# Kernel tuning notes

Hardware: AMD Instinct MI355X
Metric: run time of the kernel (lower is better)

Reference implementation:

```python
import jax, jax.numpy as jnp
from jax import lax
import numpy as np
import math

T, B, F = 512, 256, 256  # num_steps, batch, input_size == hidden_size
H = F


def setup_inputs() -> dict:
    key = jax.random.key(0)
    ks = jax.random.split(key, 20)
    stdv = 1.0 / math.sqrt(H)

    def u(k, n):
        return jax.random.uniform(k, (n,), jnp.float32, -stdv, stdv)

    X = jax.random.normal(ks[0], (T, B, F), jnp.float32)
    Mask = (jax.random.uniform(ks[1], (T, B, F)) < 0.7).astype(jnp.float32)
    Delta = jax.random.uniform(ks[2], (T, B, F), jnp.float32)

    return {
        "X": X, "Mask": Mask, "Delta": Delta,
        "x_mean": u(ks[3], F),
        "w_dg_x": u(ks[4], F), "b_dg_x": u(ks[5], F),
        "w_dg_h": u(ks[6], H), "b_dg_h": u(ks[7], H),
        "w_xz": u(ks[8], F), "u_hz": u(ks[9], H), "b_z": u(ks[10], H),
        "w_xr": u(ks[11], F), "u_hr": u(ks[12], H), "b_r": u(ks[13], H),
        "w_xh": u(ks[14], F), "u_hh": u(ks[15], H), "v_mh": u(ks[16], F),
        "b_h": u(ks[17], H),
    }


def reference(X, Mask, Delta, x_mean, w_dg_x, b_dg_x, w_dg_h, b_dg_h,
              w_xz, u_hz, b_z, w_xr, u_hr, b_r, w_xh, u_hh, v_mh, b_h):
    batch = X.shape[1]

    def step(h, inp):
        x, m, d = inp  # each [B, F]
        gamma_x = jnp.exp(-jnp.maximum(0.0, w_dg_x * d + b_dg_x))
        gamma_h = jnp.exp(-jnp.maximum(0.0, w_dg_h * d + b_dg_h))
        x = m * x + (1.0 - m) * (gamma_x * x + (1.0 - gamma_x) * x_mean)
        h = gamma_h * h
        z = jax.nn.sigmoid(w_xz * x + u_hz * h + b_z)
        r = jax.nn.sigmoid(w_xr * x + u_hr * h + b_r)
        h_tilde = jnp.tanh(w_xh * x + u_hh * (r * h) + v_mh * m + b_h)
        h = (1.0 - z) * h + z * h_tilde
        return h, h

    h0 = jnp.zeros((batch, H), X.dtype)
    _, hs = lax.scan(step, h0, (X, Mask, Delta))  # hs: [T, B, H]
    hidden_states = jnp.transpose(hs, (1, 0, 2))  # [B, T, H]
    return hidden_states, hidden_states[:, -1, :]
```

## Files before the change

### kernel.cpp

```cpp
#include <hip/hip_runtime.h>
#include <math.h>


#define TT 512
#define BB 256
#define FF 256
#define BF (BB * FF)
#define CH 8
#define NCH (TT / CH)

__device__ __forceinline__ float fast_sigmoid(float x) {
    return __builtin_amdgcn_rcpf(1.0f + __expf(-x));
}
__device__ __forceinline__ float fast_tanh(float x) {
    return fmaf(-2.0f, __builtin_amdgcn_rcpf(1.0f + __expf(2.0f * x)), 1.0f);
}

__global__ __launch_bounds__(512) void grud_kernel(
    const float* __restrict__ X, const float* __restrict__ Mask,
    const float* __restrict__ Delta,
    const float* __restrict__ x_mean,
    const float* __restrict__ w_dg_x, const float* __restrict__ b_dg_x,
    const float* __restrict__ w_dg_h, const float* __restrict__ b_dg_h,
    const float* __restrict__ w_xz, const float* __restrict__ u_hz,
    const float* __restrict__ b_z,
    const float* __restrict__ w_xr, const float* __restrict__ u_hr,
    const float* __restrict__ b_r,
    const float* __restrict__ w_xh, const float* __restrict__ u_hh,
    const float* __restrict__ v_mh, const float* __restrict__ b_h,
    float* __restrict__ out)
{
    __shared__ float lds[2][3][CH][FF];

    const int tid = threadIdx.x;
    const int blk = blockIdx.x;

    if (tid >= 256) {
        const int j = tid - 256;
        const float* srcs[3] = { X     + (size_t)blk * FF,
                                 Mask  + (size_t)blk * FF,
                                 Delta + (size_t)blk * FF };

        {
            #pragma unroll
            for (int arr = 0; arr < 3; ++arr) {
                const float* s = srcs[arr];
                #pragma unroll
                for (int i2 = 0; i2 < 2; ++i2) {
                    const int rem  = i2 * 256 + j;
                    const int step = rem >> 6;
                    const int f4   = (rem & 63) << 2;
                    *(float4*)&lds[0][arr][step][f4] =
                        *(const float4*)(s + (size_t)step * BF + f4);
                }
            }
        }
        __syncthreads();

        for (int k = 0; k < NCH; ++k) {
            if (k + 1 < NCH) {
                const int bufi = (k + 1) & 1;
                const int t0   = (k + 1) * CH;
                #pragma unroll
                for (int arr = 0; arr < 3; ++arr) {
                    const float* s = srcs[arr];
                    #pragma unroll
                    for (int i2 = 0; i2 < 2; ++i2) {
                        const int rem  = i2 * 256 + j;
                        const int step = rem >> 6;
                        const int f4   = (rem & 63) << 2;
                        *(float4*)&lds[bufi][arr][step][f4] =
                            *(const float4*)(s + (size_t)(t0 + step) * BF + f4);
                    }
                }
            }
            __syncthreads();
        }
    } else {
        const int f = tid;
        const float xm  = x_mean[f];
        const float wdx = w_dg_x[f], bdx = b_dg_x[f];
        const float wdh = w_dg_h[f], bdh = b_dg_h[f];
        const float wxz = w_xz[f],   uhz = u_hz[f], bz = b_z[f];
        const float wxr = w_xr[f],   uhr = u_hr[f], br = b_r[f];
        const float wxh = w_xh[f],   uhh = u_hh[f];
        const float vmh = v_mh[f],   bh  = b_h[f];

        float h = 0.0f;
        __syncthreads();

        for (int k = 0; k < NCH; ++k) {
            const int cb = k & 1;
            float* op = out + ((size_t)blk * TT + (size_t)k * CH) * FF + f;
            #pragma unroll
            for (int s = 0; s < CH; ++s) {
                float x = lds[cb][0][s][f];
                float m = lds[cb][1][s][f];
                float d = lds[cb][2][s][f];

                float gx = __expf(-fmaxf(0.0f, fmaf(wdx, d, bdx)));
                float gh = __expf(-fmaxf(0.0f, fmaf(wdh, d, bdh)));
                float xhat = fmaf(gx, x, (1.0f - gx) * xm);
                x = fmaf(m, x, (1.0f - m) * xhat);
                h = gh * h;
                float z  = fast_sigmoid(fmaf(wxz, x, fmaf(uhz, h, bz)));
                float r  = fast_sigmoid(fmaf(wxr, x, fmaf(uhr, h, br)));
                float ht = fast_tanh(fmaf(wxh, x, fmaf(uhh, r * h, fmaf(vmh, m, bh))));
                h = fmaf(z, ht - h, h);
                op[s * FF] = h;
            }
            __syncthreads();
        }

        out[(size_t)BB * TT * FF + (size_t)blk * FF + f] = h;
    }
}

extern "C" void kernel_launch(void* const* d_in, const int* in_sizes, int n_in,
                              void* d_out, int out_size, void* d_ws, size_t ws_size,
                              hipStream_t stream) {
    const float* X      = (const float*)d_in[0];
    const float* Mask   = (const float*)d_in[1];
    const float* Delta  = (const float*)d_in[2];
    const float* x_mean = (const float*)d_in[3];
    const float* w_dg_x = (const float*)d_in[4];
    const float* b_dg_x = (const float*)d_in[5];
    const float* w_dg_h = (const float*)d_in[6];
    const float* b_dg_h = (const float*)d_in[7];
    const float* w_xz   = (const float*)d_in[8];
    const float* u_hz   = (const float*)d_in[9];
    const float* b_z    = (const float*)d_in[10];
    const float* w_xr   = (const float*)d_in[11];
    const float* u_hr   = (const float*)d_in[12];
    const float* b_r    = (const float*)d_in[13];
    const float* w_xh   = (const float*)d_in[14];
    const float* u_hh   = (const float*)d_in[15];
    const float* v_mh   = (const float*)d_in[16];
    const float* b_h    = (const float*)d_in[17];
    float* out = (float*)d_out;

    grud_kernel<<<BB, 512, 0, stream>>>(
        X, Mask, Delta, x_mean, w_dg_x, b_dg_x, w_dg_h, b_dg_h,
        w_xz, u_hz, b_z, w_xr, u_hr, b_r, w_xh, u_hh, v_mh, b_h, out);
}
```

Before: 412.2 us.

## Replace LDS producer warps with register double-buffered direct loads

Drops the producer/consumer split that staged X/Mask/Delta through double-buffered LDS with block barriers. Each thread now loads its own feature column for two chunks of 16 steps into register arrays and alternates compute and prefetch, with no barriers. Outputs are written with nontemporal stores. This removes LDS traffic and __syncthreads, but the loads become scalar per-thread accesses (still coalesced across the wave) and register pressure rises from 96 buffered values.

After: 430.2 us. 1.04x slower.

```diff
diff --git a/kernel.cpp b/kernel.cpp
--- a/kernel.cpp
+++ b/kernel.cpp
@@ -6,7 +6,7 @@
 #define BB 256
 #define FF 256
 #define BF (BB * FF)
-#define CH 8
+#define CH 16
 #define NCH (TT / CH)
 
 __device__ __forceinline__ float fast_sigmoid(float x) {
@@ -16,7 +16,7 @@
     return fmaf(-2.0f, __builtin_amdgcn_rcpf(1.0f + __expf(2.0f * x)), 1.0f);
 }
 
-__global__ __launch_bounds__(512) void grud_kernel(
+__global__ __launch_bounds__(256, 1) void grud_kernel(
     const float* __restrict__ X, const float* __restrict__ Mask,
     const float* __restrict__ Delta,
     const float* __restrict__ x_mean,
@@ -30,90 +30,68 @@
     const float* __restrict__ v_mh, const float* __restrict__ b_h,
     float* __restrict__ out)
 {
-    __shared__ float lds[2][3][CH][FF];
+    const int f = threadIdx.x;
+    const int b = blockIdx.x;
 
-    const int tid = threadIdx.x;
-    const int blk = blockIdx.x;
+    const size_t base = (size_t)b * FF + f;
+    const float* __restrict__ px = X     + base;
+    const float* __restrict__ pm = Mask  + base;
+    const float* __restrict__ pd = Delta + base;
+    float* __restrict__ ob = out + (size_t)b * TT * FF + f;
 
-    if (tid >= 256) {
-        const int j = tid - 256;
-        const float* srcs[3] = { X     + (size_t)blk * FF,
-                                 Mask  + (size_t)blk * FF,
-                                 Delta + (size_t)blk * FF };
+    const float xm  = x_mean[f];
+    const float wdx = w_dg_x[f], bdx = b_dg_x[f];
+    const float wdh = w_dg_h[f], bdh = b_dg_h[f];
+    const float wxz = w_xz[f],   uhz = u_hz[f], bz = b_z[f];
+    const float wxr = w_xr[f],   uhr = u_hr[f], br = b_r[f];
+    const float wxh = w_xh[f],   uhh = u_hh[f];
+    const float vmh = v_mh[f],   bh  = b_h[f];
 
-        {
-            #pragma unroll
-            for (int arr = 0; arr < 3; ++arr) {
-                const float* s = srcs[arr];
-                #pragma unroll
-                for (int i2 = 0; i2 < 2; ++i2) {
-                    const int rem  = i2 * 256 + j;
-                    const int step = rem >> 6;
-                    const int f4   = (rem & 63) << 2;
-                    *(float4*)&lds[0][arr][step][f4] =
-                        *(const float4*)(s + (size_t)step * BF + f4);
-                }
-            }
+    float ax[CH], am[CH], ad[CH];
+    float ex[CH], em[CH], ed[CH];
+    float h = 0.0f;
+
+    auto loadc = [&](float (&dx)[CH], float (&dm)[CH], float (&dd)[CH], int k0) {
+        const size_t o = (size_t)k0 * CH * BF;
+        #pragma unroll
+        for (int s = 0; s < CH; ++s) dx[s] = px[o + (size_t)s * BF];
+        #pragma unroll
+        for (int s = 0; s < CH; ++s) dm[s] = pm[o + (size_t)s * BF];
+        #pragma unroll
+        for (int s = 0; s < CH; ++s) dd[s] = pd[o + (size_t)s * BF];
+    };
+
+    auto computec = [&](float (&dx)[CH], float (&dm)[CH], float (&dd)[CH], int k0) {
+        float* op = ob + (size_t)k0 * CH * FF;
+        #pragma unroll
+        for (int s = 0; s < CH; ++s) {
+            float x = dx[s], m = dm[s], d = dd[s];
+            float gx = __expf(-fmaxf(0.0f, fmaf(wdx, d, bdx)));
+            float gh = __expf(-fmaxf(0.0f, fmaf(wdh, d, bdh)));
+            float xhat = fmaf(gx, x, (1.0f - gx) * xm);
+            x = fmaf(m, x, (1.0f - m) * xhat);
+            h = gh * h;
+            float z  = fast_sigmoid(fmaf(wxz, x, fmaf(uhz, h, bz)));
+            float r  = fast_sigmoid(fmaf(wxr, x, fmaf(uhr, h, br)));
+            float ht = fast_tanh(fmaf(wxh, x, fmaf(uhh, r * h, fmaf(vmh, m, bh))));
+            h = fmaf(z, ht - h, h);
+            __builtin_nontemporal_store(h, op + (size_t)s * FF);
         }
-        __syncthreads();
+    };
 
-        for (int k = 0; k < NCH; ++k) {
-            if (k + 1 < NCH) {
-                const int bufi = (k + 1) & 1;
-                const int t0   = (k + 1) * CH;
-                #pragma unroll
-                for (int arr = 0; arr < 3; ++arr) {
-                    const float* s = srcs[arr];
-                    #pragma unroll
-                    for (int i2 = 0; i2 < 2; ++i2) {
-                        const int rem  = i2 * 256 + j;
-                        const int step = rem >> 6;
-                        const int f4   = (rem & 63) << 2;
-                        *(float4*)&lds[bufi][arr][step][f4] =
-                            *(const float4*)(s + (size_t)(t0 + step) * BF + f4);
-                    }
-                }
-            }
-            __syncthreads();
-        }
-    } else {
-        const int f = tid;
-        const float xm  = x_mean[f];
-        const float wdx = w_dg_x[f], bdx = b_dg_x[f];
-        const float wdh = w_dg_h[f], bdh = b_dg_h[f];
-        const float wxz = w_xz[f],   uhz = u_hz[f], bz = b_z[f];
-        const float wxr = w_xr[f],   uhr = u_hr[f], br = b_r[f];
-        const float wxh = w_xh[f],   uhh = u_hh[f];
-        const float vmh = v_mh[f],   bh  = b_h[f];
+    loadc(ax, am, ad, 0);
+    loadc(ex, em, ed, 1);
 
-        float h = 0.0f;
-        __syncthreads();
+    for (int k = 0; k < NCH - 2; k += 2) {
+        computec(ax, am, ad, k);
+        loadc(ax, am, ad, k + 2);
+        computec(ex, em, ed, k + 1);
+        loadc(ex, em, ed, k + 3);
+    }
+    computec(ax, am, ad, NCH - 2);
+    computec(ex, em, ed, NCH - 1);
 
-        for (int k = 0; k < NCH; ++k) {
-            const int cb = k & 1;
-            float* op = out + ((size_t)blk * TT + (size_t)k * CH) * FF + f;
-            #pragma unroll
-            for (int s = 0; s < CH; ++s) {
-                float x = lds[cb][0][s][f];
-                float m = lds[cb][1][s][f];
-                float d = lds[cb][2][s][f];
-
-                float gx = __expf(-fmaxf(0.0f, fmaf(wdx, d, bdx)));
-                float gh = __expf(-fmaxf(0.0f, fmaf(wdh, d, bdh)));
-                float xhat = fmaf(gx, x, (1.0f - gx) * xm);
-                x = fmaf(m, x, (1.0f - m) * xhat);
-                h = gh * h;
-                float z  = fast_sigmoid(fmaf(wxz, x, fmaf(uhz, h, bz)));
-                float r  = fast_sigmoid(fmaf(wxr, x, fmaf(uhr, h, br)));
-                float ht = fast_tanh(fmaf(wxh, x, fmaf(uhh, r * h, fmaf(vmh, m, bh))));
-                h = fmaf(z, ht - h, h);
-                op[s * FF] = h;
-            }
-            __syncthreads();
-        }
-
-        out[(size_t)BB * TT * FF + (size_t)blk * FF + f] = h;
-    }
+    out[(size_t)BB * TT * FF + (size_t)b * FF + f] = h;
 }
 
 extern "C" void kernel_launch(void* const* d_in, const int* in_sizes, int n_in,
@@ -139,7 +117,7 @@
     const float* b_h    = (const float*)d_in[17];
     float* out = (float*)d_out;
 
-    grud_kernel<<<BB, 512, 0, stream>>>(
+    grud_kernel<<<BB, 256, 0, stream>>>(
         X, Mask, Delta, x_mean, w_dg_x, b_dg_x, w_dg_h, b_dg_h,
         w_xz, u_hz, b_z, w_xr, u_hr, b_r, w_xh, u_hh, v_mh, b_h, out);
 }
```
